# Optimization experiments

Measured on AMD Instinct MI355X. Metric: run time of the kernel, lower is better.

## Reference

```python
import jax, jax.numpy as jnp
import numpy as np

D = 1024   # embd_dim
H = 4      # number of SelectiveAttentionModule heads (each full-dim)
B, S = 4, 2048


def _layernorm(x, g, b, eps=1e-5):
    mu = jnp.mean(x, axis=-1, keepdims=True)
    var = jnp.var(x, axis=-1, keepdims=True)
    return (x - mu) * jax.lax.rsqrt(var + eps) * g + b


def setup_inputs() -> dict:
    key = jax.random.key(0)
    ks = jax.random.split(key, 16)
    sd = 1.0 / np.sqrt(D)
    x = jax.random.normal(ks[0], (B, S, D), dtype=jnp.float32)
    # per-head Q/K/V projections, stacked over head dim H ([H, in, out] layout)
    Wq = jax.random.uniform(ks[1], (H, D, D), jnp.float32, -sd, sd)
    bq = jax.random.uniform(ks[2], (H, D), jnp.float32, -sd, sd)
    Wk = jax.random.uniform(ks[3], (H, D, D), jnp.float32, -sd, sd)
    bk = jax.random.uniform(ks[4], (H, D), jnp.float32, -sd, sd)
    Wv = jax.random.uniform(ks[5], (H, D, D), jnp.float32, -sd, sd)
    bv = jax.random.uniform(ks[6], (H, D), jnp.float32, -sd, sd)
    sd1 = 1.0 / np.sqrt(H * D)
    W1 = jax.random.uniform(ks[7], (H * D, D), jnp.float32, -sd1, sd1)  # [in, out]
    b1 = jax.random.uniform(ks[8], (D,), jnp.float32, -sd1, sd1)
    W2 = jax.random.uniform(ks[9], (D, D), jnp.float32, -sd, sd)
    b2 = jax.random.uniform(ks[10], (D,), jnp.float32, -sd, sd)
    g1 = jnp.ones((D,), jnp.float32)
    be1 = jnp.zeros((D,), jnp.float32)
    g2 = jnp.ones((D,), jnp.float32)
    be2 = jnp.zeros((D,), jnp.float32)
    return {"embedding_matrix": x, "Wq": Wq, "bq": bq, "Wk": Wk, "bk": bk,
            "Wv": Wv, "bv": bv, "W1": W1, "b1": b1, "g1": g1, "be1": be1,
            "W2": W2, "b2": b2, "g2": g2, "be2": be2}


def reference(embedding_matrix, Wq, bq, Wk, bk, Wv, bv, W1, b1, g1, be1, W2, b2, g2, be2):
    x = embedding_matrix  # [B, S, D]
    # batched per-head projections: [H, B, S, D]
    q = jnp.einsum('bsd,hde->hbse', x, Wq) + bq[:, None, None, :]
    k = jnp.einsum('bsd,hde->hbse', x, Wk) + bk[:, None, None, :]
    v = jnp.einsum('bsd,hde->hbse', x, Wv) + bv[:, None, None, :]
    scale = 1.0 / jnp.sqrt(jnp.asarray(D, x.dtype))
    scores = jnp.einsum('hbse,hbte->hbst', q, k) * scale  # [H, B, S, S]
    attn = jax.nn.softmax(scores, axis=-1)
    heads = jnp.einsum('hbst,hbte->hbse', attn, v)        # [H, B, S, D]
    # torch.cat([V1..V4], dim=-1) == heads reordered to [B, S, H*D]
    concat = jnp.moveaxis(heads, 0, 2).reshape(x.shape[0], x.shape[1], H * D)
    proj = concat @ W1 + b1                               # [B, S, D]
    y = _layernorm(x + proj, g1, be1)
    return _layernorm(y + (y @ W2 + b2), g2, be2)
```

## Files before the change

kernel.cpp:

```cpp
#include <hip/hip_runtime.h>

using u16 = unsigned short;
using u32 = unsigned int;
typedef __attribute__((ext_vector_type(8))) short s16x8;
typedef __attribute__((ext_vector_type(4))) float f32x4;

typedef uint4   __attribute__((may_alias)) uint4a;
typedef ushort4 __attribute__((may_alias)) ushort4a;
typedef float4  __attribute__((may_alias)) float4a;
typedef u16     __attribute__((may_alias)) u16a;
typedef s16x8   __attribute__((may_alias)) s16x8a;

#define D_ 1024
#define H_ 4
#define B_ 4
#define S_ 2048
#define M_ 8192

#define BM 128
#define BN 128
#define BK 32

__device__ __forceinline__ float bf2f(u16 u) { return __uint_as_float(((u32)u) << 16); }
__device__ __forceinline__ u16 f2bf(float f) {
  u32 b = __float_as_uint(f);
  return (u16)((b + 0x7fffu + ((b >> 16) & 1u)) >> 16);
}

__device__ __forceinline__ void gload_lds16(const u16* g, u16* l) {
  __builtin_amdgcn_global_load_lds(
      (const __attribute__((address_space(1))) void*)g,
      (__attribute__((address_space(3))) void*)l, 16, 0, 0);
}

#define FENCE asm volatile("" ::: "memory")
#define BAR do { FENCE; __builtin_amdgcn_s_barrier(); FENCE; } while (0)
#define VMC4 asm volatile("s_waitcnt vmcnt(4)" ::: "memory")

__device__ __forceinline__ void swz_decomp(int& x, int& y, int& z) {
  const int gx = gridDim.x, gy = gridDim.y;
  const int nwg = gx * gy * gridDim.z;
  const int flat = (blockIdx.z * gy + blockIdx.y) * gx + blockIdx.x;
  const int swz = (flat & 7) * (nwg >> 3) + (flat >> 3);
  const int t = swz >> 4, i = swz & 15;
  const int tiles_X = (gx * gridDim.z) >> 2;
  const int X = (t % tiles_X) * 4 + (i & 3);
  y = (t / tiles_X) * 4 + (i >> 2);
  z = X / gx;
  x = X % gx;
}

__global__ __launch_bounds__(256) void cvt_f32_bf16(const float* __restrict__ in,
                                                    u16* __restrict__ out, long n4) {
  long stride = (long)gridDim.x * blockDim.x;
  for (long i = (long)blockIdx.x * blockDim.x + threadIdx.x; i < n4; i += stride) {
    float4 v = ((const float4a*)in)[i];
    ushort4 o;
    o.x = f2bf(v.x); o.y = f2bf(v.y); o.z = f2bf(v.z); o.w = f2bf(v.w);
    ((ushort4a*)out)[i] = o;
  }
}

__global__ __launch_bounds__(256) void tcvt(const float* __restrict__ in,
                                            u16* __restrict__ out, int K, int N,
                                            long s_in, long s_out) {
  __shared__ float t[32][33];
  const int z = blockIdx.z;
  in += (long)z * s_in;
  out += (long)z * s_out;
  const int n0 = blockIdx.x * 32, k0 = blockIdx.y * 32;
  const int tx = threadIdx.x & 31, ty = threadIdx.x >> 5;
#pragma unroll
  for (int i = 0; i < 32; i += 8) t[ty + i][tx] = in[(long)(k0 + ty + i) * N + n0 + tx];
  __syncthreads();
#pragma unroll
  for (int i = 0; i < 32; i += 8)
    out[(long)(n0 + ty + i) * K + k0 + tx] = f2bf(t[tx][ty + i]);
}

__global__ __launch_bounds__(256) void biascat(const float* __restrict__ bq,
                                               const float* __restrict__ bk,
                                               const float* __restrict__ bv,
                                               float* __restrict__ o) {
  int i = blockIdx.x * 256 + threadIdx.x;
  float v = (i < 4096) ? bq[i] : ((i < 8192) ? bk[i - 4096] : bv[i - 8192]);
  o[i] = v;
}

__global__ __launch_bounds__(256) void dred(const float* __restrict__ dpart,
                                            float* __restrict__ drow) {
  int t = blockIdx.x * 256 + threadIdx.x;
  int z = t >> 11, row = t & 2047;
  float s = 0.f;
#pragma unroll
  for (int p = 0; p < 32; ++p) s += dpart[((long)z * 32 + p) * 2048 + row];
  drow[t] = s;
}

__device__ __forceinline__ s16x8 lds_frag(const u16* buf, int r, int jc) {
  return *(const s16x8a*)&buf[(((r << 3) + (jc ^ (r & 7)))) << 3];
}
__device__ __forceinline__ void readB(const u16* Bbuf, int wc, int lane, s16x8 (&bfr)[4][2]) {
#pragma unroll
  for (int j = 0; j < 4; ++j)
#pragma unroll
    for (int s = 0; s < 2; ++s)
      bfr[j][s] = lds_frag(Bbuf, wc * 64 + j * 16 + (lane & 15), 4 * s + (lane >> 4));
}
__device__ __forceinline__ void readA(const u16* Abuf, int q, int wr, int lane, s16x8 (&afr)[2][2]) {
#pragma unroll
  for (int il = 0; il < 2; ++il)
#pragma unroll
    for (int s = 0; s < 2; ++s)
      afr[il][s] = lds_frag(Abuf, wr * 128 + (q * 2 + il) * 16 + (lane & 15), 4 * s + (lane >> 4));
}
__device__ __forceinline__ void mfma_quad(const s16x8 (&afr)[2][2], const s16x8 (&bfr)[4][2],
                                          f32x4 (&acc)[8][4], int q) {
  __builtin_amdgcn_s_setprio(1);
#pragma unroll
  for (int s = 0; s < 2; ++s)
#pragma unroll
    for (int il = 0; il < 2; ++il)
#pragma unroll
      for (int j = 0; j < 4; ++j)
        acc[q * 2 + il][j] =
            __builtin_amdgcn_mfma_f32_16x16x32_bf16(afr[il][s], bfr[j][s], acc[q * 2 + il][j], 0, 0, 0);
  __builtin_amdgcn_s_setprio(0);
}

__global__ __launch_bounds__(512, 2) void gemm256x(
    const u16* __restrict__ A, const u16* __restrict__ Bm, u16* __restrict__ Cp,
    float* __restrict__ dpart) {
  __shared__ u16 Al[2][16384];
  __shared__ u16 Bl[2][16384];
  const int flat = (blockIdx.z * 8 + blockIdx.y) * 8 + blockIdx.x;
  const int swz = (flat & 7) * 32 + (flat >> 3);
  const int bx = swz & 7, by = (swz >> 3) & 7, z = swz >> 6;
  A += (long)z * ((long)S_ * D_);
  Bm += (long)z * ((long)S_ * D_);
  const long coff = (long)z * S_ * S_;
  const int bm = by * 256, bn = bx * 256;
  const int tid = threadIdx.x;
  const int lane = tid & 63;
  const int w = tid >> 6;
  const int wr = w >> 2, wc = w & 3;
  f32x4 acc[8][4] = {};
  const int nt2 = D_ >> 7;

  auto stage = [&](const u16* src, int b0, u16* lbuf, int h, int kt) {
    const int k0 = kt << 6;
#pragma unroll
    for (int it = 0; it < 2; ++it) {
      int c = w * 128 + it * 64 + lane;
      int row = h * 128 + (c >> 3);
      int j = (c & 7) ^ (row & 7);
      gload_lds16(src + (long)(b0 + row) * D_ + (k0 + j * 8),
                  lbuf + ((h * 1024 + w * 128 + it * 64) << 3));
    }
  };

  stage(A, bm, Al[0], 0, 0);
  stage(A, bm, Al[0], 1, 0);
  stage(Bm, bn, Bl[0], 0, 0);
  stage(Bm, bn, Bl[0], 1, 0);
  stage(Bm, bn, Bl[1], 0, 1);
  stage(Bm, bn, Bl[1], 1, 1);
  VMC4;
  BAR;

  s16x8 bfr[4][2];
  for (int i2 = 0; i2 < nt2; ++i2) {
    const int t = i2 * 2;
    s16x8 afr[2][2];
    readB(Bl[0], wc, lane, bfr);
    readA(Al[0], 0, wr, lane, afr);
    stage(A, bm, Al[1], 0, t + 1);
    BAR;
    mfma_quad(afr, bfr, acc, 0);
    BAR;
    readA(Al[0], 1, wr, lane, afr);
    stage(A, bm, Al[1], 1, t + 1);
    BAR;
    mfma_quad(afr, bfr, acc, 1);
    BAR;
    readA(Al[0], 2, wr, lane, afr);
    stage(Bm, bn, Bl[0], 0, t + 2);
    BAR;
    mfma_quad(afr, bfr, acc, 2);
    BAR;
    readA(Al[0], 3, wr, lane, afr);
    stage(Bm, bn, Bl[0], 1, t + 2);
    BAR;
    mfma_quad(afr, bfr, acc, 3);
    VMC4;
    BAR;
    readB(Bl[1], wc, lane, bfr);
    readA(Al[1], 0, wr, lane, afr);
    stage(A, bm, Al[0], 0, t + 2);
    BAR;
    mfma_quad(afr, bfr, acc, 0);
    BAR;
    readA(Al[1], 1, wr, lane, afr);
    stage(A, bm, Al[0], 1, t + 2);
    BAR;
    mfma_quad(afr, bfr, acc, 1);
    BAR;
    readA(Al[1], 2, wr, lane, afr);
    stage(Bm, bn, Bl[1], 0, t + 3);
    BAR;
    mfma_quad(afr, bfr, acc, 2);
    BAR;
    readA(Al[1], 3, wr, lane, afr);
    stage(Bm, bn, Bl[1], 1, t + 3);
    BAR;
    mfma_quad(afr, bfr, acc, 3);
    VMC4;
    BAR;
  }

#pragma unroll
  for (int i = 0; i < 8; i++) {
    int mbase = bm + wr * 128 + i * 16 + ((lane >> 4) << 2);
#pragma unroll
    for (int r = 0; r < 4; r++) {
      const int mm = mbase + r;
      float rowsum = 0.f;
#pragma unroll
      for (int j = 0; j < 4; j++) {
        int n = bn + wc * 64 + j * 16 + (lane & 15);
        float e = __expf(acc[i][j][r] * 0.03125f);
        ((u16a*)Cp)[coff + (long)mm * S_ + n] = f2bf(e);
        rowsum += e;
      }
      rowsum += __shfl_xor(rowsum, 1, 64);
      rowsum += __shfl_xor(rowsum, 2, 64);
      rowsum += __shfl_xor(rowsum, 4, 64);
      rowsum += __shfl_xor(rowsum, 8, 64);
      if ((lane & 15) == 0)
        dpart[((long)z * 32 + (bx * 4 + wc)) * S_ + mm] = rowsum;
    }
  }
}

__device__ __forceinline__ int lds_slot(int row, int ks) {
  return row * 4 + (ks ^ ((row >> 1) & 3));
}

template <int OUT_MODE, int HAS_BIAS, int ACC>
__global__ __launch_bounds__(256, 4) void gemm_bt(
    const u16* __restrict__ A, const u16* __restrict__ Bm, void* __restrict__ Cp,
    const float* __restrict__ bias, float* __restrict__ drow,
    int K, int lda, int ldb, int ldc,
    long sA, long sB, long sC, long sBias, float scale) {
  __shared__ u16 Al[2][BM * BK];
  __shared__ u16 Bl[2][BN * BK];
  int bx, by, z;
  swz_decomp(bx, by, z);
  A += (long)z * sA;
  Bm += (long)z * sB;
  const long coff = (long)z * sC;
  const int bm = by * BM, bn = bx * BN;
  const int tid = threadIdx.x;
  const int lane = tid & 63;
  const int w = tid >> 6;
  const int wr = w >> 1, wc = w & 1;
  f32x4 acc[4][4] = {};

  auto stage = [&](u16* Ad, u16* Bd, int k0) {
#pragma unroll
    for (int it = 0; it < 2; ++it) {
      const int sbase = w * 128 + it * 64;
      const int slot = sbase + lane;
      const int row = slot >> 2;
      const int j = (slot & 3) ^ ((row >> 1) & 3);
      gload_lds16(A + (long)(bm + row) * lda + (k0 + j * 8), Ad + sbase * 8);
      gload_lds16(Bm + (long)(bn + row) * ldb + (k0 + j * 8), Bd + sbase * 8);
    }
  };

  stage(Al[0], Bl[0], 0);
  __syncthreads();
  int cur = 0;
  for (int k0 = 0; k0 < K; k0 += BK) {
    const int nxt = cur ^ 1;
    if (k0 + BK < K) stage(Al[nxt], Bl[nxt], k0 + BK);
    const int ks = lane >> 4;
    s16x8 a[4], b[4];
#pragma unroll
    for (int i = 0; i < 4; i++) {
      int row = wr * 64 + i * 16 + (lane & 15);
      a[i] = *(const s16x8a*)&Al[cur][lds_slot(row, ks) * 8];
    }
#pragma unroll
    for (int j = 0; j < 4; j++) {
      int row = wc * 64 + j * 16 + (lane & 15);
      b[j] = *(const s16x8a*)&Bl[cur][lds_slot(row, ks) * 8];
    }
#pragma unroll
    for (int i = 0; i < 4; i++)
#pragma unroll
      for (int j = 0; j < 4; j++)
        acc[i][j] = __builtin_amdgcn_mfma_f32_16x16x32_bf16(a[i], b[j], acc[i][j], 0, 0, 0);
    __syncthreads();
    cur = nxt;
  }

  if (OUT_MODE == 5) {
#pragma unroll
    for (int i = 0; i < 4; i++) {
      int mbase = bm + wr * 64 + i * 16 + ((lane >> 4) << 2);
      float inv[4];
#pragma unroll
      for (int r = 0; r < 4; r++) inv[r] = 1.0f / drow[(long)z * S_ + mbase + r];
#pragma unroll
      for (int j = 0; j < 4; j++) {
        int n = bn + wc * 64 + j * 16 + (lane & 15);
#pragma unroll
        for (int r = 0; r < 4; r++) {
          ((u16a*)Cp)[coff + (long)(mbase + r) * ldc + n] = f2bf(acc[i][j][r] * inv[r]);
        }
      }
    }
    return;
  }
  const bool tpose = (OUT_MODE == 3 && z == 2);
#pragma unroll
  for (int i = 0; i < 4; i++) {
    int mbase = bm + wr * 64 + i * 16 + ((lane >> 4) << 2);
#pragma unroll
    for (int j = 0; j < 4; j++) {
      int n = bn + wc * 64 + j * 16 + (lane & 15);
      float bv = 0.f;
      if (HAS_BIAS) bv = bias[z * sBias + n];
      if (tpose) {
        ushort4 o;
        o.x = f2bf(acc[i][j][0] * scale + bv);
        o.y = f2bf(acc[i][j][1] * scale + bv);
        o.z = f2bf(acc[i][j][2] * scale + bv);
        o.w = f2bf(acc[i][j][3] * scale + bv);
        long idx = coff + (long)(mbase >> 11) * ((long)D_ * S_) + (long)n * S_ + (mbase & 2047);
        *(ushort4a*)&((u16a*)Cp)[idx] = o;
      } else {
#pragma unroll
        for (int r = 0; r < 4; r++) {
          float v = acc[i][j][r] * scale + bv;
          long idx = coff + (long)(mbase + r) * ldc + n;
          if (OUT_MODE == 1 || OUT_MODE == 3) {
            ((u16a*)Cp)[idx] = f2bf(v);
          } else {
            float* Cf = (float*)Cp;
            Cf[idx] = ACC ? (Cf[idx] + v) : v;
          }
        }
      }
    }
  }
}

__global__ __launch_bounds__(256) void ln_kernel(
    const float* __restrict__ X, const float* __restrict__ R,
    const float* __restrict__ g, const float* __restrict__ be,
    float* __restrict__ Y, u16* __restrict__ Yb) {
  const long row = blockIdx.x;
  const int t = threadIdx.x, lane = t & 63, w = t >> 6;
  const long base = row * 1024 + t * 4;
  float4 a = *(const float4a*)(X + base);
  float4 b = *(const float4a*)(R + base);
  float v0 = a.x + b.x, v1 = a.y + b.y, v2 = a.z + b.z, v3 = a.w + b.w;
  float s = v0 + v1 + v2 + v3;
  float q = v0 * v0 + v1 * v1 + v2 * v2 + v3 * v3;
#pragma unroll
  for (int o = 32; o > 0; o >>= 1) { s += __shfl_xor(s, o, 64); q += __shfl_xor(q, o, 64); }
  __shared__ float rs[4], rq[4];
  if (lane == 0) { rs[w] = s; rq[w] = q; }
  __syncthreads();
  s = rs[0] + rs[1] + rs[2] + rs[3];
  q = rq[0] + rq[1] + rq[2] + rq[3];
  const float mu = s * (1.f / 1024.f);
  const float var = q * (1.f / 1024.f) - mu * mu;
  const float rstd = rsqrtf(var + 1e-5f);
  float4 gv = *(const float4a*)(g + t * 4);
  float4 bv = *(const float4a*)(be + t * 4);
  float o0 = (v0 - mu) * rstd * gv.x + bv.x;
  float o1 = (v1 - mu) * rstd * gv.y + bv.y;
  float o2 = (v2 - mu) * rstd * gv.z + bv.z;
  float o3 = (v3 - mu) * rstd * gv.w + bv.w;
  float4 o4; o4.x = o0; o4.y = o1; o4.z = o2; o4.w = o3;
  *(float4a*)(Y + base) = o4;
  if (Yb) {
    ushort4 ob; ob.x = f2bf(o0); ob.y = f2bf(o1); ob.z = f2bf(o2); ob.w = f2bf(o3);
    *(ushort4a*)(Yb + base) = ob;
  }
}

extern "C" void kernel_launch(void* const* d_in, const int* in_sizes, int n_in,
                              void* d_out, int out_size, void* d_ws, size_t ws_size,
                              hipStream_t stream) {
  const float* x   = (const float*)d_in[0];
  const float* Wq  = (const float*)d_in[1];
  const float* bq  = (const float*)d_in[2];
  const float* Wk  = (const float*)d_in[3];
  const float* bk  = (const float*)d_in[4];
  const float* Wv  = (const float*)d_in[5];
  const float* bv  = (const float*)d_in[6];
  const float* W1  = (const float*)d_in[7];
  const float* b1  = (const float*)d_in[8];
  const float* g1  = (const float*)d_in[9];
  const float* be1 = (const float*)d_in[10];
  const float* W2  = (const float*)d_in[11];
  const float* b2  = (const float*)d_in[12];
  const float* g2  = (const float*)d_in[13];
  const float* be2 = (const float*)d_in[14];
  float* out = (float*)d_out;

  const size_t NEED_BASE = 186646528ULL;
  const size_t NEED_CC   = 203423744ULL;
  if (ws_size < NEED_BASE) return;
  const bool useCc = (ws_size >= NEED_CC);
  char* ws = (char*)d_ws;
  u16* xb  = (u16*)(ws + 0L);
  u16* Wqt = (u16*)(ws + 16777216L);
  u16* Wkt = (u16*)(ws + 25165824L);
  u16* Wvt = (u16*)(ws + 33554432L);
  u16* W1t = (u16*)(ws + 41943040L);
  u16* W2t = (u16*)(ws + 50331648L);
  u16* Qh  = (u16*)(ws + 52428800L);
  u16* Kh  = (u16*)(ws + 69206016L);
  u16* Vt  = (u16*)(ws + 85983232L);
  u16* Sbh = (u16*)(ws + 102760448L);
  u16* Cc   = (u16*)(ws + 136314880L);
  u16* Ch   = (u16*)(ws + 136314880L);
  float* proj = useCc ? (float*)Sbh : (float*)(ws + 153092096L);
  float* y  = (float*)Qh;
  u16*   yb = Vt;
  float* z2 = useCc ? (float*)Cc : proj;
  float* biasQKV = out;
  float* dsum  = out + 16384;
  float* dpart = out + 65536;

  dim3 blk(256);
  {
    long n4 = (long)M_ * D_ / 4;
    hipLaunchKernelGGL(cvt_f32_bf16, dim3(4096), blk, 0, stream, x, xb, n4);
  }
  hipLaunchKernelGGL(tcvt, dim3(32, 32, H_), blk, 0, stream, Wq, Wqt, D_, D_,
                     (long)D_ * D_, (long)D_ * D_);
  hipLaunchKernelGGL(tcvt, dim3(32, 32, H_), blk, 0, stream, Wk, Wkt, D_, D_,
                     (long)D_ * D_, (long)D_ * D_);
  hipLaunchKernelGGL(tcvt, dim3(32, 32, H_), blk, 0, stream, Wv, Wvt, D_, D_,
                     (long)D_ * D_, (long)D_ * D_);
  hipLaunchKernelGGL(tcvt, dim3(32, 128, 1), blk, 0, stream, W1, W1t, H_ * D_, D_, 0L, 0L);
  hipLaunchKernelGGL(tcvt, dim3(32, 32, 1), blk, 0, stream, W2, W2t, D_, D_, 0L, 0L);
  hipLaunchKernelGGL(biascat, dim3(48), blk, 0, stream, bq, bk, bv, biasQKV);

  for (int h = 0; h < H_; ++h) {
    const long wo = (long)h * D_ * D_;
    hipLaunchKernelGGL((gemm_bt<3, 1, 0>), dim3(8, 64, 3), blk, 0, stream,
                       xb, Wqt + wo, (void*)Qh, biasQKV + (long)h * D_, (float*)nullptr,
                       D_, D_, D_, D_,
                       0L, (long)H_ * D_ * D_, (long)M_ * D_, (long)H_ * D_, 1.0f);
    hipLaunchKernelGGL(gemm256x, dim3(8, 8, B_), dim3(512), 0, stream,
                       Qh, Kh, Sbh, dpart);
    hipLaunchKernelGGL(dred, dim3(32), blk, 0, stream, dpart, dsum);
    if (useCc) {
      hipLaunchKernelGGL((gemm_bt<5, 0, 0>), dim3(8, 16, B_), blk, 0, stream,
                         Sbh, Vt, (void*)(Cc + (long)h * D_), (const float*)nullptr, dsum,
                         S_, S_, S_, H_ * D_,
                         (long)S_ * S_, (long)D_ * S_, (long)S_ * H_ * D_, 0L, 1.0f);
    } else {
      hipLaunchKernelGGL((gemm_bt<5, 0, 0>), dim3(8, 16, B_), blk, 0, stream,
                         Sbh, Vt, (void*)Ch, (const float*)nullptr, dsum,
                         S_, S_, S_, D_,
                         (long)S_ * S_, (long)D_ * S_, (long)S_ * D_, 0L, 1.0f);
      if (h == 0) {
        hipLaunchKernelGGL((gemm_bt<0, 1, 0>), dim3(8, 64, 1), blk, 0, stream,
                           Ch, W1t + (long)h * D_, (void*)proj, b1, (float*)nullptr,
                           D_, D_, H_ * D_, D_, 0L, 0L, 0L, 0L, 1.0f);
      } else {
        hipLaunchKernelGGL((gemm_bt<0, 0, 1>), dim3(8, 64, 1), blk, 0, stream,
                           Ch, W1t + (long)h * D_, (void*)proj, (const float*)nullptr,
                           (float*)nullptr, D_, D_, H_ * D_, D_, 0L, 0L, 0L, 0L, 1.0f);
      }
    }
  }

  if (useCc) {
    hipLaunchKernelGGL((gemm_bt<0, 1, 0>), dim3(8, 64, 1), blk, 0, stream,
                       Cc, W1t, (void*)proj, b1, (float*)nullptr,
                       H_ * D_, H_ * D_, H_ * D_, D_, 0L, 0L, 0L, 0L, 1.0f);
  }

  hipLaunchKernelGGL(ln_kernel, dim3(M_), blk, 0, stream, x, proj, g1, be1, y, yb);

  hipLaunchKernelGGL((gemm_bt<0, 1, 0>), dim3(8, 64, 1), blk, 0, stream,
                     yb, W2t, (void*)z2, b2, (float*)nullptr,
                     D_, D_, D_, D_, 0L, 0L, 0L, 0L, 1.0f);

  hipLaunchKernelGGL(ln_kernel, dim3(M_), blk, 0, stream, y, z2, g2, be2, out, (u16*)nullptr);
}
```

Baseline: 821.1 us.

## Run Q/K projections through the 256x256 GEMM kernel and split off the V projection

Turns the 256x256-tile GEMM into a template with two modes: a bias-add bf16 output mode used for the Q and K projections, and the existing exp/rowsum mode used for the scores. The V projection, which writes transposed output, moves to its own launch of the 128-tile GEMM. The aim is higher MFMA efficiency and more operand reuse on the large projection GEMMs. In exchange it drops the block-index swizzle from the scores kernel, which may hurt L2 locality, and adds one kernel launch per head.

```diff
diff --git a/kernel.cpp b/kernel.cpp
--- a/kernel.cpp
+++ b/kernel.cpp
@@ -128,17 +128,17 @@
   __builtin_amdgcn_s_setprio(0);
 }
 
-__global__ __launch_bounds__(512, 2) void gemm256x(
+template <int MODE>
+__global__ __launch_bounds__(512, 2) void g256(
     const u16* __restrict__ A, const u16* __restrict__ Bm, u16* __restrict__ Cp,
-    float* __restrict__ dpart) {
+    const float* __restrict__ bias, const float* __restrict__ bias2,
+    float* __restrict__ dpart, int ldc, long sA, long sB, long sC) {
   __shared__ u16 Al[2][16384];
   __shared__ u16 Bl[2][16384];
-  const int flat = (blockIdx.z * 8 + blockIdx.y) * 8 + blockIdx.x;
-  const int swz = (flat & 7) * 32 + (flat >> 3);
-  const int bx = swz & 7, by = (swz >> 3) & 7, z = swz >> 6;
-  A += (long)z * ((long)S_ * D_);
-  Bm += (long)z * ((long)S_ * D_);
-  const long coff = (long)z * S_ * S_;
+  const int bx = blockIdx.x, by = blockIdx.y, z = blockIdx.z;
+  A += (long)z * sA;
+  Bm += (long)z * sB;
+  const long coff = (long)z * sC;
   const int bm = by * 256, bn = bx * 256;
   const int tid = threadIdx.x;
   const int lane = tid & 63;
@@ -218,26 +218,42 @@
     BAR;
   }
 
-#pragma unroll
-  for (int i = 0; i < 8; i++) {
-    int mbase = bm + wr * 128 + i * 16 + ((lane >> 4) << 2);
-#pragma unroll
-    for (int r = 0; r < 4; r++) {
-      const int mm = mbase + r;
-      float rowsum = 0.f;
+  if (MODE == 0) {
+    const float* bb = (z == 1) ? bias2 : bias;
+#pragma unroll
+    for (int i = 0; i < 8; i++) {
+      int mbase = bm + wr * 128 + i * 16 + ((lane >> 4) << 2);
 #pragma unroll
       for (int j = 0; j < 4; j++) {
         int n = bn + wc * 64 + j * 16 + (lane & 15);
-        float e = __expf(acc[i][j][r] * 0.03125f);
-        ((u16a*)Cp)[coff + (long)mm * S_ + n] = f2bf(e);
-        rowsum += e;
+        float bv = bb[n];
+#pragma unroll
+        for (int r = 0; r < 4; r++)
+          ((u16a*)Cp)[coff + (long)(mbase + r) * ldc + n] = f2bf(acc[i][j][r] + bv);
       }
-      rowsum += __shfl_xor(rowsum, 1, 64);
-      rowsum += __shfl_xor(rowsum, 2, 64);
-      rowsum += __shfl_xor(rowsum, 4, 64);
-      rowsum += __shfl_xor(rowsum, 8, 64);
-      if ((lane & 15) == 0)
-        dpart[((long)z * 32 + (bx * 4 + wc)) * S_ + mm] = rowsum;
+    }
+  } else {
+#pragma unroll
+    for (int i = 0; i < 8; i++) {
+      int mbase = bm + wr * 128 + i * 16 + ((lane >> 4) << 2);
+#pragma unroll
+      for (int r = 0; r < 4; r++) {
+        const int mm = mbase + r;
+        float rowsum = 0.f;
+#pragma unroll
+        for (int j = 0; j < 4; j++) {
+          int n = bn + wc * 64 + j * 16 + (lane & 15);
+          float e = __expf(acc[i][j][r] * 0.03125f);
+          ((u16a*)Cp)[coff + (long)mm * ldc + n] = f2bf(e);
+          rowsum += e;
+        }
+        rowsum += __shfl_xor(rowsum, 1, 64);
+        rowsum += __shfl_xor(rowsum, 2, 64);
+        rowsum += __shfl_xor(rowsum, 4, 64);
+        rowsum += __shfl_xor(rowsum, 8, 64);
+        if ((lane & 15) == 0)
+          dpart[((long)z * 32 + (bx * 4 + wc)) * S_ + mm] = rowsum;
+      }
     }
   }
 }
@@ -323,7 +339,6 @@
     }
     return;
   }
-  const bool tpose = (OUT_MODE == 3 && z == 2);
 #pragma unroll
   for (int i = 0; i < 4; i++) {
     int mbase = bm + wr * 64 + i * 16 + ((lane >> 4) << 2);
@@ -332,7 +347,7 @@
       int n = bn + wc * 64 + j * 16 + (lane & 15);
       float bv = 0.f;
       if (HAS_BIAS) bv = bias[z * sBias + n];
-      if (tpose) {
+      if (OUT_MODE == 2) {
         ushort4 o;
         o.x = f2bf(acc[i][j][0] * scale + bv);
         o.y = f2bf(acc[i][j][1] * scale + bv);
@@ -345,7 +360,7 @@
         for (int r = 0; r < 4; r++) {
           float v = acc[i][j][r] * scale + bv;
           long idx = coff + (long)(mbase + r) * ldc + n;
-          if (OUT_MODE == 1 || OUT_MODE == 3) {
+          if (OUT_MODE == 1) {
             ((u16a*)Cp)[idx] = f2bf(v);
           } else {
             float* Cf = (float*)Cp;
@@ -455,12 +470,16 @@
 
   for (int h = 0; h < H_; ++h) {
     const long wo = (long)h * D_ * D_;
-    hipLaunchKernelGGL((gemm_bt<3, 1, 0>), dim3(8, 64, 3), blk, 0, stream,
-                       xb, Wqt + wo, (void*)Qh, biasQKV + (long)h * D_, (float*)nullptr,
-                       D_, D_, D_, D_,
-                       0L, (long)H_ * D_ * D_, (long)M_ * D_, (long)H_ * D_, 1.0f);
-    hipLaunchKernelGGL(gemm256x, dim3(8, 8, B_), dim3(512), 0, stream,
-                       Qh, Kh, Sbh, dpart);
+    hipLaunchKernelGGL((g256<0>), dim3(4, 32, 2), dim3(512), 0, stream,
+                       xb, Wqt + wo, Qh, biasQKV + (long)h * D_,
+                       biasQKV + 4096 + (long)h * D_, (float*)nullptr,
+                       D_, 0L, (long)H_ * D_ * D_, (long)M_ * D_);
+    hipLaunchKernelGGL((gemm_bt<2, 1, 0>), dim3(8, 64, 1), blk, 0, stream,
+                       xb, Wvt + wo, (void*)Vt, biasQKV + 8192 + (long)h * D_,
+                       (float*)nullptr, D_, D_, D_, D_, 0L, 0L, 0L, 0L, 1.0f);
+    hipLaunchKernelGGL((g256<1>), dim3(8, 8, B_), dim3(512), 0, stream,
+                       Qh, Kh, Sbh, (const float*)nullptr, (const float*)nullptr,
+                       dpart, S_, (long)S_ * D_, (long)S_ * D_, (long)S_ * S_);
     hipLaunchKernelGGL(dred, dim3(32), blk, 0, stream, dpart, dsum);
     if (useCc) {
       hipLaunchKernelGGL((gemm_bt<5, 0, 0>), dim3(8, 16, B_), blk, 0, stream,
```

Result: no change. 823.4 us (+0.3%).
